# Performance work log

Hardware: AMD Instinct MI355X
Metric: run time of the kernel (lower is better)

## Reference

```python
import jax, jax.numpy as jnp
import numpy as np

P, V, D = 1024, 49408, 512


def setup_inputs() -> dict:
    key = jax.random.key(0)
    k1, k2 = jax.random.split(key)
    prompt_embs = jax.random.normal(k1, (P, D), dtype=jnp.float32)
    clip_embs = jax.random.normal(k2, (V, D), dtype=jnp.float32)
    return {"prompt_embs": prompt_embs, "clip_embs": clip_embs}


def reference(prompt_embs, clip_embs):
    # torch.cdist(p=2): Euclidean distance matrix [P, V].
    # ||a-b||^2 = ||a||^2 + ||b||^2 - 2 a.b ; sqrt is monotone so argmin of
    # the (clamped) squared distance matches argmin of the true distance.
    a2 = jnp.sum(prompt_embs * prompt_embs, axis=-1, keepdims=True)   # [P,1]
    b2 = jnp.sum(clip_embs * clip_embs, axis=-1)                      # [V]
    ab = jnp.einsum("pd,vd->pv", prompt_embs, clip_embs)              # [P,V]
    d2 = jnp.maximum(a2 + b2[None, :] - 2.0 * ab, 0.0)                # [P,V]
    prompt_ids = jnp.argmin(d2, axis=1)                               # [P]
    new_embs = clip_embs[prompt_ids]                                  # [P,D] gather
    return new_embs, prompt_ids
```

## Files before the change

### kernel.cpp

```cpp
#include <hip/hip_runtime.h>
#include <stdint.h>

#define NP 1024
#define NV 49408
#define ND 512
#define NTILE 48

typedef __attribute__((ext_vector_type(8))) __bf16 bf16x8;
typedef __attribute__((ext_vector_type(4))) float f32x4;

__device__ inline unsigned long long pack_sv(float s, unsigned v) {
  unsigned u = __float_as_uint(s);
  u = (u & 0x80000000u) ? ~u : (u | 0x80000000u);
  return ((unsigned long long)u << 32) | (unsigned long long)v;
}

__global__ __launch_bounds__(256) void pack_rows_k(const float* __restrict__ src,
                                                   __bf16* __restrict__ dst,
                                                   float* __restrict__ sumsq,
                                                   int nrows) {
  int lane = threadIdx.x & 63;
  int row = blockIdx.x * 4 + (threadIdx.x >> 6);
  if (row >= nrows) return;
  const float* r = src + (size_t)row * ND + lane * 8;
  float4 x0 = *(const float4*)r;
  float4 x1 = *(const float4*)(r + 4);
  float xs[8] = {x0.x, x0.y, x0.z, x0.w, x1.x, x1.y, x1.z, x1.w};
  bf16x8 hi, lo;
  float ss = 0.f;
#pragma unroll
  for (int j = 0; j < 8; ++j) {
    float x = xs[j];
    ss += x * x;
    __bf16 h = (__bf16)x;
    hi[j] = h;
    lo[j] = (__bf16)(x - (float)h);
  }
  __bf16* drow = dst + (size_t)row * 1024 + lane * 8;
  *(bf16x8*)drow = hi;
  *(bf16x8*)(drow + 512) = lo;
  if (sumsq != nullptr) {
#pragma unroll
    for (int m = 1; m < 64; m <<= 1) ss += __shfl_xor(ss, m);
    if (lane == 0) sumsq[row] = ss;
  }
}


__device__ __attribute__((always_inline)) static inline
void gll16(const char* src, char* dst) {
  __builtin_amdgcn_global_load_lds(
      (const __attribute__((address_space(1))) void*)src,
      (__attribute__((address_space(3))) void*)dst, 16, 0, 0);
}

template <int R>
__device__ __attribute__((always_inline)) static inline
void phase_op(f32x4 (&acc)[4][4], const char* aBase, const char* bBase,
              const char* sA, const char* sB, char* st) {
  constexpr int RS = (R + 2) % 3;
#pragma unroll
  for (int i = 0; i < 2; ++i) gll16(sA + i * 131072, st + RS * 16384 + i * 4096);
#pragma unroll
  for (int i = 0; i < 2; ++i) gll16(sB + i * 131072, st + RS * 16384 + 8192 + i * 4096);
  bf16x8 a[4], b[4];
#pragma unroll
  for (int m = 0; m < 4; ++m) a[m] = *(const bf16x8*)(aBase + R * 16384 + m * 1024);
#pragma unroll
  for (int n = 0; n < 4; ++n) b[n] = *(const bf16x8*)(bBase + R * 16384 + n * 1024);
  asm volatile("" ::: "memory");
  __builtin_amdgcn_s_barrier();
  asm volatile("" ::: "memory");
  __builtin_amdgcn_s_setprio(1);
#pragma unroll
  for (int m = 0; m < 4; ++m)
#pragma unroll
    for (int n = 0; n < 4; ++n)
      acc[m][n] = __builtin_amdgcn_mfma_f32_16x16x32_bf16(a[m], b[n], acc[m][n], 0, 0, 0);
  __builtin_amdgcn_s_setprio(0);
  asm volatile("s_waitcnt vmcnt(4)" ::: "memory");
  __builtin_amdgcn_s_barrier();
  asm volatile("" ::: "memory");
}

__global__ __launch_bounds__(256, 3) void gemm_argmin_k(const __bf16* __restrict__ A,
                                                        const __bf16* __restrict__ B,
                                                        const float* __restrict__ b2,
                                                        unsigned long long* __restrict__ best) {
  __shared__ __align__(16) char lds[49152];
  const int tid = threadIdx.x;
  const int lane = tid & 63;
  const int wid = tid >> 6;
  const int wm = wid >> 1;
  const int wn = wid & 1;

  const int d = blockIdx.x;
  const int o = (d & 7) * 386 + (d >> 3);
  const int bm = (o & 7) * 128;
  const int bn = (o >> 3) * 128;

  const int r = lane & 15, g = lane >> 4;
  const int rh = r >> 1;
  const int laneByte = rh * 128 + (r & 1) * 64 + (((g + rh) & 3) << 4);
  const char* aBase = (const char*)lds + wm * 4096 + laneByte;
  const char* bBase = (const char*)lds + 8192 + wn * 4096 + laneByte;

  const int srow0 = 2 * (tid >> 3) + ((tid >> 2) & 1);
  const int sc16 = ((tid & 3) - (tid >> 3)) & 3;
  const char* srcA = (const char*)A + (size_t)(bm + srow0) * 2048 + sc16 * 16;
  const char* srcB = (const char*)B + (size_t)(bn + srow0) * 2048 + sc16 * 16;
  char* st = (char*)lds + tid * 16;

  f32x4 acc[4][4] = {};

  auto aByte = [](int t) { return (t & 31) * 64; };
  auto bByte = [](int t) { return (t & 15) * 64 + (t >= 32 ? 1024 : 0); };

#pragma unroll
  for (int i = 0; i < 2; ++i) gll16(srcA + aByte(0) + i * 131072, st + i * 4096);
#pragma unroll
  for (int i = 0; i < 2; ++i) gll16(srcB + bByte(0) + i * 131072, st + 8192 + i * 4096);
#pragma unroll
  for (int i = 0; i < 2; ++i) gll16(srcA + aByte(1) + i * 131072, st + 16384 + i * 4096);
#pragma unroll
  for (int i = 0; i < 2; ++i) gll16(srcB + bByte(1) + i * 131072, st + 16384 + 8192 + i * 4096);
  asm volatile("s_waitcnt vmcnt(4)" ::: "memory");
  __builtin_amdgcn_s_barrier();
  asm volatile("" ::: "memory");

#pragma unroll 1
  for (int it = 0; it < 16; ++it) {
    const int p = 3 * it;
    int t2 = p + 2; if (t2 >= NTILE) t2 -= NTILE;
    int t3 = p + 3; if (t3 >= NTILE) t3 -= NTILE;
    int t4 = p + 4; if (t4 >= NTILE) t4 -= NTILE;
    phase_op<0>(acc, aBase, bBase, srcA + aByte(t2), srcB + bByte(t2), st);
    phase_op<1>(acc, aBase, bBase, srcA + aByte(t3), srcB + bByte(t3), st);
    phase_op<2>(acc, aBase, bBase, srcA + aByte(t4), srcB + bByte(t4), st);
  }

  float bb[4];
#pragma unroll
  for (int n = 0; n < 4; ++n) bb[n] = b2[bn + wn * 64 + n * 16 + r];
#pragma unroll
  for (int m = 0; m < 4; ++m) {
#pragma unroll
    for (int reg = 0; reg < 4; ++reg) {
      unsigned long long pk = ~0ull;
#pragma unroll
      for (int n = 0; n < 4; ++n) {
        float s = bb[n] - 2.0f * acc[m][n][reg];
        unsigned long long cand = pack_sv(s, (unsigned)(bn + wn * 64 + n * 16 + r));
        pk = (cand < pk) ? cand : pk;
      }
#pragma unroll
      for (int msk = 1; msk < 16; msk <<= 1) {
        unsigned long long o2 = __shfl_xor(pk, msk);
        pk = (o2 < pk) ? o2 : pk;
      }
      if (r == 0) atomicMin(&best[bm + wm * 64 + m * 16 + g * 4 + reg], pk);
    }
  }
}

__global__ __launch_bounds__(256) void naive_argmin_k(const float* __restrict__ A,
                                                      const float* __restrict__ B,
                                                      unsigned long long* __restrict__ best) {
  __shared__ float arow[ND];
  int p = blockIdx.y;
  unsigned v = blockIdx.x * 256 + threadIdx.x;
  for (int i = threadIdx.x; i < ND; i += 256) arow[i] = A[(size_t)p * ND + i];
  __syncthreads();
  const float4* br = (const float4*)(B + (size_t)v * ND);
  float s = 0.f;
#pragma unroll 4
  for (int i = 0; i < ND / 4; ++i) {
    float4 b = br[i];
    const float4 a = *(const float4*)&arow[i * 4];
    float d0 = a.x - b.x, d1 = a.y - b.y, d2 = a.z - b.z, d3 = a.w - b.w;
    s += d0 * d0 + d1 * d1 + d2 * d2 + d3 * d3;
  }
  unsigned long long pk = pack_sv(s, v);
#pragma unroll
  for (int msk = 1; msk < 64; msk <<= 1) {
    unsigned long long o = __shfl_xor(pk, msk);
    pk = (o < pk) ? o : pk;
  }
  if ((threadIdx.x & 63) == 0) atomicMin(&best[p], pk);
}

__global__ __launch_bounds__(128) void gather_k(const unsigned long long* __restrict__ best,
                                                const float* __restrict__ clip,
                                                float* __restrict__ out) {
  int p = blockIdx.x;
  unsigned long long pk = best[p];
  unsigned v = (unsigned)(pk & 0xffffffffull);
  const float4* src = (const float4*)(clip + (size_t)v * ND);
  float4* dst = (float4*)(out + (size_t)p * ND);
  dst[threadIdx.x] = src[threadIdx.x];
  if (threadIdx.x == 0) out[(size_t)NP * ND + p] = (float)v;
}

extern "C" void kernel_launch(void* const* d_in, const int* in_sizes, int n_in,
                              void* d_out, int out_size, void* d_ws, size_t ws_size,
                              hipStream_t stream) {
  const float* prompt = (const float*)d_in[0];
  const float* clip = (const float*)d_in[1];
  float* out = (float*)d_out;

  size_t off = 0;
  unsigned long long* best = (unsigned long long*)d_ws;
  off += (size_t)NP * 8;
  float* b2 = (float*)((char*)d_ws + off);
  off += (size_t)NV * 4;
  off = (off + 255) & ~(size_t)255;
  __bf16* Ap = (__bf16*)((char*)d_ws + off);
  off += (size_t)NP * 1024 * 2;
  __bf16* Bp = (__bf16*)((char*)d_ws + off);
  off += (size_t)NV * 1024 * 2;
  const size_t need = off;

  if (ws_size >= need) {
    hipMemsetAsync(best, 0xFF, (size_t)NP * 8, stream);
    pack_rows_k<<<NP / 4, 256, 0, stream>>>(prompt, Ap, nullptr, NP);
    pack_rows_k<<<NV / 4, 256, 0, stream>>>(clip, Bp, b2, NV);
    gemm_argmin_k<<<dim3(8 * 386), 256, 0, stream>>>(Ap, Bp, b2, best);
    gather_k<<<NP, 128, 0, stream>>>(best, clip, out);
  } else {
    hipMemsetAsync(best, 0xFF, (size_t)NP * 8, stream);
    dim3 grid(NV / 256, NP);
    naive_argmin_k<<<grid, 256, 0, stream>>>(prompt, clip, best);
    gather_k<<<NP, 128, 0, stream>>>(best, clip, out);
  }
}
```

Measured before the change: 229.9 us.

## Load A fragments directly from global into registers, stage only B in LDS

```diff
diff --git a/kernel.cpp b/kernel.cpp
--- a/kernel.cpp
+++ b/kernel.cpp
@@ -8,6 +8,7 @@
 
 typedef __attribute__((ext_vector_type(8))) __bf16 bf16x8;
 typedef __attribute__((ext_vector_type(4))) float f32x4;
+typedef __attribute__((ext_vector_type(4))) int i32x4;
 
 __device__ inline unsigned long long pack_sv(float s, unsigned v) {
   unsigned u = __float_as_uint(s);
@@ -54,40 +55,55 @@
       (__attribute__((address_space(3))) void*)dst, 16, 0, 0);
 }
 
-template <int R>
 __device__ __attribute__((always_inline)) static inline
-void phase_op(f32x4 (&acc)[4][4], const char* aBase, const char* bBase,
-              const char* sA, const char* sB, char* st) {
-  constexpr int RS = (R + 2) % 3;
-#pragma unroll
-  for (int i = 0; i < 2; ++i) gll16(sA + i * 131072, st + RS * 16384 + i * 4096);
-#pragma unroll
-  for (int i = 0; i < 2; ++i) gll16(sB + i * 131072, st + RS * 16384 + 8192 + i * 4096);
-  bf16x8 a[4], b[4];
-#pragma unroll
-  for (int m = 0; m < 4; ++m) a[m] = *(const bf16x8*)(aBase + R * 16384 + m * 1024);
-#pragma unroll
-  for (int n = 0; n < 4; ++n) b[n] = *(const bf16x8*)(bBase + R * 16384 + n * 1024);
-  asm volatile("" ::: "memory");
+bf16x8 lds_read(unsigned addr) {
+  i32x4 d;
+  asm volatile("ds_read_b128 %0, %1" : "=v"(d) : "v"(addr));
+  return __builtin_bit_cast(bf16x8, d);
+}
+
+#define FENCE asm volatile("" ::: "memory")
+
+template <int PH>
+__device__ __attribute__((always_inline)) static inline
+void phase_op(f32x4 (&acc)[4][4], bf16x8 (&aE)[4], bf16x8 (&aO)[4],
+              const char* Ab, const int (&voffA)[4],
+              const char* srcBt, char* stB, unsigned bRead, int p) {
+  constexpr int R = PH % 3;
+  constexpr int RS = (PH + 2) % 3;
+  const int kA = ((p + 1) & 31) * 64;
+  const int t2 = p + 2;
+  const int kB = (t2 & 15) * 64 + (t2 >= 32 ? 1024 : 0);
+  bf16x8 (&aN)[4] = (PH % 2 == 0) ? aO : aE;
+  bf16x8 (&aC)[4] = (PH % 2 == 0) ? aE : aO;
+#pragma unroll
+  for (int m = 0; m < 4; ++m)
+    aN[m] = *(const bf16x8*)(Ab + voffA[m] + kA);
+  gll16(srcBt + kB, stB + RS * 8192);
+  gll16(srcBt + kB + 131072, stB + RS * 8192 + 4096);
+  bf16x8 b[4];
+#pragma unroll
+  for (int n = 0; n < 4; ++n)
+    b[n] = lds_read(bRead + R * 8192 + n * 1024);
+  asm volatile("s_waitcnt vmcnt(6) lgkmcnt(0)" ::: "memory");
+  __builtin_amdgcn_sched_barrier(0);
+  __builtin_amdgcn_s_setprio(1);
+#pragma unroll
+  for (int m = 0; m < 4; ++m)
+#pragma unroll
+    for (int n = 0; n < 4; ++n)
+      acc[m][n] = __builtin_amdgcn_mfma_f32_16x16x32_bf16(aC[m], b[n], acc[m][n], 0, 0, 0);
+  __builtin_amdgcn_s_setprio(0);
+  FENCE;
   __builtin_amdgcn_s_barrier();
-  asm volatile("" ::: "memory");
-  __builtin_amdgcn_s_setprio(1);
-#pragma unroll
-  for (int m = 0; m < 4; ++m)
-#pragma unroll
-    for (int n = 0; n < 4; ++n)
-      acc[m][n] = __builtin_amdgcn_mfma_f32_16x16x32_bf16(a[m], b[n], acc[m][n], 0, 0, 0);
-  __builtin_amdgcn_s_setprio(0);
-  asm volatile("s_waitcnt vmcnt(4)" ::: "memory");
-  __builtin_amdgcn_s_barrier();
-  asm volatile("" ::: "memory");
-}
-
-__global__ __launch_bounds__(256, 3) void gemm_argmin_k(const __bf16* __restrict__ A,
+  FENCE;
+}
+
+__global__ __launch_bounds__(256, 4) void gemm_argmin_k(const __bf16* __restrict__ A,
                                                         const __bf16* __restrict__ B,
                                                         const float* __restrict__ b2,
                                                         unsigned long long* __restrict__ best) {
-  __shared__ __align__(16) char lds[49152];
+  __shared__ __align__(16) char lds[24576];
   const int tid = threadIdx.x;
   const int lane = tid & 63;
   const int wid = tid >> 6;
@@ -101,42 +117,44 @@
 
   const int r = lane & 15, g = lane >> 4;
   const int rh = r >> 1;
-  const int laneByte = rh * 128 + (r & 1) * 64 + (((g + rh) & 3) << 4);
-  const char* aBase = (const char*)lds + wm * 4096 + laneByte;
-  const char* bBase = (const char*)lds + 8192 + wn * 4096 + laneByte;
-
-  const int srow0 = 2 * (tid >> 3) + ((tid >> 2) & 1);
+  const unsigned lds0 =
+      (unsigned)(uintptr_t)(const __attribute__((address_space(3))) char*)(const char*)lds;
+  const unsigned bRead = lds0 + wn * 4096 + rh * 128 + (r & 1) * 64 + (((g + rh) & 3) << 4);
+
+  const char* Ab = (const char*)A + (size_t)bm * 2048;
+  int voffA[4];
+#pragma unroll
+  for (int m = 0; m < 4; ++m) voffA[m] = (wm * 64 + m * 16 + r) * 2048 + g * 16;
+
+  const int srow = 2 * (tid >> 3) + ((tid >> 2) & 1);
   const int sc16 = ((tid & 3) - (tid >> 3)) & 3;
-  const char* srcA = (const char*)A + (size_t)(bm + srow0) * 2048 + sc16 * 16;
-  const char* srcB = (const char*)B + (size_t)(bn + srow0) * 2048 + sc16 * 16;
-  char* st = (char*)lds + tid * 16;
+  const char* srcBt = (const char*)B + (size_t)(bn + srow) * 2048 + sc16 * 16;
+  char* stB = (char*)lds + tid * 16;
 
   f32x4 acc[4][4] = {};
-
-  auto aByte = [](int t) { return (t & 31) * 64; };
-  auto bByte = [](int t) { return (t & 15) * 64 + (t >= 32 ? 1024 : 0); };
-
-#pragma unroll
-  for (int i = 0; i < 2; ++i) gll16(srcA + aByte(0) + i * 131072, st + i * 4096);
-#pragma unroll
-  for (int i = 0; i < 2; ++i) gll16(srcB + bByte(0) + i * 131072, st + 8192 + i * 4096);
-#pragma unroll
-  for (int i = 0; i < 2; ++i) gll16(srcA + aByte(1) + i * 131072, st + 16384 + i * 4096);
-#pragma unroll
-  for (int i = 0; i < 2; ++i) gll16(srcB + bByte(1) + i * 131072, st + 16384 + 8192 + i * 4096);
-  asm volatile("s_waitcnt vmcnt(4)" ::: "memory");
+  bf16x8 aE[4], aO[4];
+
+#pragma unroll
+  for (int m = 0; m < 4; ++m)
+    aE[m] = *(const bf16x8*)(Ab + voffA[m] + 0);
+  gll16(srcBt + 0, stB + 0);
+  gll16(srcBt + 0 + 131072, stB + 4096);
+  gll16(srcBt + 64, stB + 8192);
+  gll16(srcBt + 64 + 131072, stB + 8192 + 4096);
+  asm volatile("s_waitcnt vmcnt(2)" ::: "memory");
+  FENCE;
   __builtin_amdgcn_s_barrier();
-  asm volatile("" ::: "memory");
+  FENCE;
 
 #pragma unroll 1
-  for (int it = 0; it < 16; ++it) {
-    const int p = 3 * it;
-    int t2 = p + 2; if (t2 >= NTILE) t2 -= NTILE;
-    int t3 = p + 3; if (t3 >= NTILE) t3 -= NTILE;
-    int t4 = p + 4; if (t4 >= NTILE) t4 -= NTILE;
-    phase_op<0>(acc, aBase, bBase, srcA + aByte(t2), srcB + bByte(t2), st);
-    phase_op<1>(acc, aBase, bBase, srcA + aByte(t3), srcB + bByte(t3), st);
-    phase_op<2>(acc, aBase, bBase, srcA + aByte(t4), srcB + bByte(t4), st);
+  for (int it = 0; it < 8; ++it) {
+    const int p0 = 6 * it;
+    phase_op<0>(acc, aE, aO, Ab, voffA, srcBt, stB, bRead, p0 + 0);
+    phase_op<1>(acc, aE, aO, Ab, voffA, srcBt, stB, bRead, p0 + 1);
+    phase_op<2>(acc, aE, aO, Ab, voffA, srcBt, stB, bRead, p0 + 2);
+    phase_op<3>(acc, aE, aO, Ab, voffA, srcBt, stB, bRead, p0 + 3);
+    phase_op<4>(acc, aE, aO, Ab, voffA, srcBt, stB, bRead, p0 + 4);
+    phase_op<5>(acc, aE, aO, Ab, voffA, srcBt, stB, bRead, p0 + 5);
   }
 
   float bb[4];
```

Result: slower. 834.8 us (+263.2%).
